# Performance work log

Measured on AMD Instinct MI355X. Metric: run time of the kernel, lower is better.

Reference implementation:

```python
import jax, jax.numpy as jnp
import numpy as np

IMG_H, IMG_W = 448, 800
GRID = 224
MIN_SIZE = 64.0
B, N, NCAM = 1, 48, 6


def setup_inputs() -> dict:
    rng = np.random.default_rng(0)
    centers = np.stack([rng.uniform(-40, 40, (B, N)), rng.uniform(-40, 40, (B, N)),
                        rng.uniform(-1.5, 0.5, (B, N))], -1)
    dims = rng.uniform(1.0, 4.0, (B, N, 3))
    heading = rng.uniform(-np.pi, np.pi, (B, N, 1))
    boxes7 = np.concatenate([centers, dims, heading], -1).astype(np.float32)
    gt_labels = rng.integers(1, 11, (B, N)).astype(np.int64)  # 1..10 as in gt_boxes[...,-1]
    imgs = rng.random((B, NCAM, 3, IMG_H, IMG_W)).astype(np.float32)
    # plausible lidar->image projections: 6 outward-facing cams, 60 deg apart, 90 deg hfov
    fx = fy = 400.0
    K = np.array([[fx, 0, IMG_W / 2], [0, fy, IMG_H / 2], [0, 0, 1]], np.float32)
    l2i = np.zeros((B, NCAM, 4, 4), np.float32)
    for c in range(NCAM):
        th = 2 * np.pi * c / NCAM
        right = np.array([np.sin(th), -np.cos(th), 0.0])
        down = np.array([0.0, 0.0, -1.0])
        fwdv = np.array([np.cos(th), np.sin(th), 0.0])
        R = np.stack([right, down, fwdv])  # lidar -> cam
        l2i[:, c, :3, :3] = K @ R
        l2i[:, c, 3, 3] = 1.0
    eye4 = np.eye(4, dtype=np.float32)
    img_aug = np.broadcast_to(eye4, (B, NCAM, 4, 4)).copy()
    lidar_aug = np.broadcast_to(eye4, (B, 4, 4)).copy()
    W_img = (rng.standard_normal((588, 768)) * 0.02).astype(np.float32)
    text_features = rng.standard_normal((10, 768)).astype(np.float32)
    return dict(boxes7=jnp.asarray(boxes7), gt_labels=jnp.asarray(gt_labels),
                camera_imgs=jnp.asarray(imgs), lidar2image=jnp.asarray(l2i),
                img_aug_matrix=jnp.asarray(img_aug), lidar_aug_matrix=jnp.asarray(lidar_aug),
                W_img=jnp.asarray(W_img), text_features=jnp.asarray(text_features),
                logit_scale=jnp.asarray(np.float32(np.log(100.0))))


def _boxes_to_corners_3d(boxes7):  # (M,7) -> (M,8,3)
    template = jnp.array([[1, 1, -1], [1, -1, -1], [-1, -1, -1], [-1, 1, -1],
                          [1, 1, 1], [1, -1, 1], [-1, -1, 1], [-1, 1, 1]], jnp.float32) * 0.5
    corners = boxes7[:, None, 3:6] * template[None]
    c, s = jnp.cos(boxes7[:, 6]), jnp.sin(boxes7[:, 6])
    z, o = jnp.zeros_like(c), jnp.ones_like(c)
    rot = jnp.stack([c, s, z, -s, c, z, z, z, o], -1).reshape(-1, 3, 3)
    corners = jnp.einsum('nki,nij->nkj', corners, rot)  # points @ R as in torch code
    return corners + boxes7[:, None, :3]


def _project(corners, l2i, img_aug, lidar_aug):
    # corners (M,3); l2i/img_aug (6,4,4); lidar_aug (4,4)
    pts = corners - lidar_aug[:3, 3]
    pts = jnp.linalg.inv(lidar_aug[:3, :3]) @ pts.T  # (3,M)
    p = jnp.einsum('cij,jm->cim', l2i[:, :3, :3], pts) + l2i[:, :3, 3][:, :, None]
    zc = jnp.clip(p[:, 2], 1e-5, 1e5)
    xy = p[:, :2] / zc[:, None]
    p = jnp.concatenate([xy, zc[:, None]], axis=1)  # (6,3,M)
    p = jnp.einsum('cij,cjm->cim', img_aug[:, :3, :3], p) + img_aug[:, :3, 3][:, :, None]
    rc = p[:, :2].transpose(0, 2, 1)[..., ::-1]  # (6,M,2) as (row, col)
    on_img = (rc[..., 0] < IMG_H) & (rc[..., 0] >= 0) & (rc[..., 1] < IMG_W) & (rc[..., 1] >= 0)
    return rc, on_img


def _bilinear(img, ix, iy):
    # img (3,H,W); ix, iy (N,GRID,GRID) pixel coords; zero padding, align_corners=False
    x0f, y0f = jnp.floor(ix), jnp.floor(iy)
    wx1, wy1 = ix - x0f, iy - y0f
    wx0, wy0 = 1.0 - wx1, 1.0 - wy1

    def gather(xf, yf):
        valid = (xf >= 0) & (xf <= IMG_W - 1) & (yf >= 0) & (yf <= IMG_H - 1)
        xi = jnp.clip(xf.astype(jnp.int32), 0, IMG_W - 1)
        yi = jnp.clip(yf.astype(jnp.int32), 0, IMG_H - 1)
        return img[:, yi, xi] * valid[None].astype(img.dtype)  # (3,N,G,G)

    return (gather(x0f, y0f) * (wx0 * wy0)[None] + gather(x0f + 1, y0f) * (wx1 * wy0)[None]
            + gather(x0f, y0f + 1) * (wx0 * wy1)[None] + gather(x0f + 1, y0f + 1) * (wx1 * wy1)[None])


def _forward(boxes7, gt_labels, camera_imgs, lidar2image, img_aug_matrix,
             lidar_aug_matrix, W_img, text_features, logit_scale):
    Bx, Nx = boxes7.shape[:2]
    corners = _boxes_to_corners_3d(boxes7.reshape(-1, 7)).reshape(Bx, Nx * 8, 3)
    rc, on_img = jax.vmap(_project)(corners, lidar2image, img_aug_matrix, lidar_aug_matrix)
    # .long() in torch truncates toward zero; coords are constants wrt grads
    all_coords = jax.lax.stop_gradient(jnp.trunc(rc)).astype(jnp.int32).reshape(Bx, NCAM, Nx, 8, 2)
    visible = on_img.reshape(Bx, NCAM, Nx, 8).any(-1)  # (B,6,N)
    rows, cols = all_coords[..., 0], all_coords[..., 1]
    x1 = jnp.clip(cols.min(-1), 0, IMG_W)
    x2 = jnp.clip(cols.max(-1), 0, IMG_W)
    y1 = jnp.clip(rows.min(-1), 0, IMG_H)
    y2 = jnp.clip(rows.max(-1), 0, IMG_H)
    sq = jnp.maximum(jnp.maximum(x2 - x1, y2 - y1).astype(jnp.float32), MIN_SIZE)
    u = jnp.linspace(0.0, 1.0, GRID)  # normalized affine_grid after min/max rescale
    px = x1.astype(jnp.float32)[..., None, None] + sq[..., None, None] * u[None, None, None, None, :]
    py = y1.astype(jnp.float32)[..., None, None] + sq[..., None, None] * u[None, None, None, :, None]
    gx = px / IMG_W * 2.0 - 1.0
    gy = py / IMG_H * 2.0 - 1.0
    ix = ((gx + 1.0) * IMG_W - 1.0) / 2.0  # unnormalize (align_corners=False)
    iy = ((gy + 1.0) * IMG_H - 1.0) / 2.0
    patches = jax.vmap(jax.vmap(_bilinear))(camera_imgs, ix, iy)  # (B,6,3,N,G,G)
    patches = patches.transpose(0, 1, 3, 2, 4, 5)  # (B,6,N,3,G,G)
    # stub CLIP image tower: 16x16 avg pool -> flatten -> linear to 768
    pooled = patches.reshape(Bx, NCAM, Nx, 3, 14, 16, 14, 16).mean(axis=(5, 7))
    feats = pooled.reshape(Bx, NCAM, Nx, 588) @ W_img  # (B,6,N,768)
    feats = feats / jnp.linalg.norm(feats, axis=-1, keepdims=True)
    text_n = text_features / jnp.linalg.norm(text_features, axis=-1, keepdims=True)
    logits = jnp.exp(logit_scale) * jnp.einsum('bcnd,kd->bcnk', feats, text_n)
    probs = jax.nn.softmax(logits, axis=-1) * visible[..., None].astype(logits.dtype)
    cnt = visible.sum(1).astype(probs.dtype)  # (B,N) cameras per box
    mean_probs = probs.sum(1) / jnp.maximum(cnt, 1.0)[..., None]  # (B,N,10)
    pred = jnp.argmax(mean_probs, axis=-1).reshape(-1)
    true = gt_labels.reshape(-1) - 1
    acc = (pred == true).astype(jnp.float32).mean()
    return pred, true, acc, mean_probs


def reference(boxes7, gt_labels, camera_imgs, lidar2image, img_aug_matrix,
              lidar_aug_matrix, W_img, text_features, logit_scale):
    return _forward(boxes7, gt_labels, camera_imgs, lidar2image, img_aug_matrix,
                    lidar_aug_matrix, W_img, text_features, logit_scale)
```

## Files before the change

kernel.cpp:

```cpp
#include <hip/hip_runtime.h>
#include <math.h>

#define IMG_H 448
#define IMG_W 800
#define GRIDN 224
#define NCAM 6
#define NBOX 48
#define NPAIR (NCAM * NBOX)
#define NCLASS 10
#define FEATD 768
#define POOLD 588
#define PROWS 14

#define WS_PAIR 0
#define WS_PART (NPAIR * 4)
#define WS_PROBS (WS_PART + NPAIR * PROWS * FEATD)

__global__ void __launch_bounds__(256) pool_gemv_kernel(const float* __restrict__ imgs,
                                                        const float* __restrict__ boxes7,
                                                        const float* __restrict__ l2i,
                                                        const float* __restrict__ img_aug,
                                                        const float* __restrict__ lidar_aug,
                                                        const float* __restrict__ W,
                                                        float* __restrict__ ws) {
    int pair = blockIdx.x / PROWS;
    int pr = blockIdx.x % PROWS;
    int cam = pair / NBOX, box = pair % NBOX;
    int tid = threadIdx.x;

    __shared__ float s_pw[4];
    __shared__ float s_pool[3 * 14];

    if (tid < 8) {
        int k = tid;
        float R[9];
        for (int i = 0; i < 3; ++i)
            for (int j = 0; j < 3; ++j) R[i * 3 + j] = lidar_aug[i * 4 + j];
        float ltx = lidar_aug[3], lty = lidar_aug[7], ltz = lidar_aug[11];
        float det = R[0] * (R[4] * R[8] - R[5] * R[7]) - R[1] * (R[3] * R[8] - R[5] * R[6]) +
                    R[2] * (R[3] * R[7] - R[4] * R[6]);
        float i0 = (R[4] * R[8] - R[5] * R[7]) / det;
        float i1 = (R[2] * R[7] - R[1] * R[8]) / det;
        float i2 = (R[1] * R[5] - R[2] * R[4]) / det;
        float i3 = (R[5] * R[6] - R[3] * R[8]) / det;
        float i4 = (R[0] * R[8] - R[2] * R[6]) / det;
        float i5 = (R[2] * R[3] - R[0] * R[5]) / det;
        float i6 = (R[3] * R[7] - R[4] * R[6]) / det;
        float i7 = (R[1] * R[6] - R[0] * R[7]) / det;
        float i8 = (R[0] * R[4] - R[1] * R[3]) / det;

        const float* M = l2i + cam * 16;
        const float* A = img_aug + cam * 16;
        const float* bxp = boxes7 + box * 7;
        float cx = bxp[0], cy = bxp[1], cz = bxp[2];
        float dx = bxp[3], dy = bxp[4], dz = bxp[5], hd = bxp[6];
        float ch = cosf(hd), sh = sinf(hd);
        float tx = (k & 2) ? -0.5f : 0.5f;
        float ty = ((k + 1) & 2) ? -0.5f : 0.5f;
        float tz = (k & 4) ? 0.5f : -0.5f;
        float lx = dx * tx, ly = dy * ty, lz = dz * tz;
        float wx = lx * ch - ly * sh + cx;
        float wy = lx * sh + ly * ch + cy;
        float wz = lz + cz;
        float px_ = wx - ltx, py_ = wy - lty, pz_ = wz - ltz;
        float qx = i0 * px_ + i1 * py_ + i2 * pz_;
        float qy = i3 * px_ + i4 * py_ + i5 * pz_;
        float qz = i6 * px_ + i7 * py_ + i8 * pz_;
        float p0 = M[0] * qx + M[1] * qy + M[2] * qz + M[3];
        float p1 = M[4] * qx + M[5] * qy + M[6] * qz + M[7];
        float p2 = M[8] * qx + M[9] * qy + M[10] * qz + M[11];
        float zc = fminf(fmaxf(p2, 1e-5f), 1e5f);
        float sx = p0 / zc, sy = p1 / zc;
        float q0 = A[0] * sx + A[1] * sy + A[2] * zc + A[3];
        float q1 = A[4] * sx + A[5] * sy + A[6] * zc + A[7];
        float row = q1, col = q0;
        int on = (row < (float)IMG_H) && (row >= 0.f) && (col < (float)IMG_W) && (col >= 0.f);
        int ri = (int)row;
        int ci = (int)col;
        int minr = ri, maxr = ri, minc = ci, maxc = ci, visv = on;
        for (int off = 4; off >= 1; off >>= 1) {
            minr = min(minr, __shfl_xor(minr, off, 8));
            maxr = max(maxr, __shfl_xor(maxr, off, 8));
            minc = min(minc, __shfl_xor(minc, off, 8));
            maxc = max(maxc, __shfl_xor(maxc, off, 8));
            visv |= __shfl_xor(visv, off, 8);
        }
        if (tid == 0) {
            int x1 = min(max(minc, 0), IMG_W);
            int x2 = min(max(maxc, 0), IMG_W);
            int y1 = min(max(minr, 0), IMG_H);
            int y2 = min(max(maxr, 0), IMG_H);
            float sq = fmaxf((float)max(x2 - x1, y2 - y1), 64.0f);
            s_pw[0] = (float)x1;
            s_pw[1] = (float)y1;
            s_pw[2] = sq;
            s_pw[3] = visv ? 1.0f : 0.0f;
            if (pr == 0) {
                float* pw = ws + WS_PAIR + pair * 4;
                pw[0] = (float)x1; pw[1] = (float)y1; pw[2] = sq;
                pw[3] = visv ? 1.0f : 0.0f;
            }
        }
    }
    __syncthreads();
    if (s_pw[3] == 0.f) return;
    float bx1 = s_pw[0], by1 = s_pw[1], sq = s_pw[2];

    const float* img0 = imgs + (size_t)cam * 3 * IMG_H * IMG_W;
    const float* img1 = img0 + (size_t)(IMG_H * IMG_W);
    const float* img2 = img0 + (size_t)(2 * IMG_H * IMG_W);
    bool active = tid < GRIDN;

    const float ustep = 1.0f / 223.0f;
    float wx0 = 0.f, wx1 = 0.f, mx0 = 0.f, mx1 = 0.f;
    int xi0 = 0, xi1 = 0;
    if (active) {
        float u = (float)tid * ustep;
        float px = bx1 + sq * u;
        float gx = px / (float)IMG_W * 2.0f - 1.0f;
        float ix = ((gx + 1.0f) * (float)IMG_W - 1.0f) / 2.0f;
        float x0f = floorf(ix);
        wx1 = ix - x0f;
        wx0 = 1.0f - wx1;
        float x1f = x0f + 1.0f;
        mx0 = (x0f >= 0.f && x0f <= (float)(IMG_W - 1)) ? 1.f : 0.f;
        mx1 = (x1f >= 0.f && x1f <= (float)(IMG_W - 1)) ? 1.f : 0.f;
        xi0 = min(max((int)x0f, 0), IMG_W - 1);
        xi1 = min(max((int)x1f, 0), IMG_W - 1);
    }

    int iyA = -0x40000000, iyB = -0x40000000;
    float vA00 = 0.f, vA01 = 0.f, vA10 = 0.f, vA11 = 0.f, vA20 = 0.f, vA21 = 0.f;
    float vB00 = 0.f, vB01 = 0.f, vB10 = 0.f, vB11 = 0.f, vB20 = 0.f, vB21 = 0.f;

    float acc0 = 0.f, acc1 = 0.f, acc2 = 0.f;
    for (int r = 0; r < 16; ++r) {
        int i = pr * 16 + r;
        float u = (float)i * ustep;
        float py = by1 + sq * u;
        float gy = py / (float)IMG_H * 2.0f - 1.0f;
        float iy = ((gy + 1.0f) * (float)IMG_H - 1.0f) / 2.0f;
        float y0f = floorf(iy);
        float wy1 = iy - y0f;
        float wy0 = 1.0f - wy1;
        float y1f = y0f + 1.0f;
        float my0 = (y0f >= 0.f && y0f <= (float)(IMG_H - 1)) ? 1.f : 0.f;
        float my1 = (y1f >= 0.f && y1f <= (float)(IMG_H - 1)) ? 1.f : 0.f;
        int yi0 = min(max((int)y0f, 0), IMG_H - 1);
        int yi1 = min(max((int)y1f, 0), IMG_H - 1);
        if (yi0 != iyA || yi1 != iyB) {
            if (yi0 == iyB) {
                vA00 = vB00; vA01 = vB01; vA10 = vB10; vA11 = vB11; vA20 = vB20; vA21 = vB21;
                iyA = iyB;
            } else if (yi0 != iyA) {
                if (active) {
                    int r0 = yi0 * IMG_W;
                    vA00 = img0[r0 + xi0]; vA01 = img0[r0 + xi1];
                    vA10 = img1[r0 + xi0]; vA11 = img1[r0 + xi1];
                    vA20 = img2[r0 + xi0]; vA21 = img2[r0 + xi1];
                }
                iyA = yi0;
            }
            if (yi1 != iyB) {
                if (active) {
                    int r1 = yi1 * IMG_W;
                    vB00 = img0[r1 + xi0]; vB01 = img0[r1 + xi1];
                    vB10 = img1[r1 + xi0]; vB11 = img1[r1 + xi1];
                    vB20 = img2[r1 + xi0]; vB21 = img2[r1 + xi1];
                }
                iyB = yi1;
            }
        }
        if (active) {
            float w00 = wx0 * wy0, w10 = wx1 * wy0, w01 = wx0 * wy1, w11 = wx1 * wy1;
            float m00 = mx0 * my0, m10 = mx1 * my0, m01 = mx0 * my1, m11 = mx1 * my1;
            acc0 += vA00 * m00 * w00 + vA01 * m10 * w10 + vB00 * m01 * w01 + vB01 * m11 * w11;
            acc1 += vA10 * m00 * w00 + vA11 * m10 * w10 + vB10 * m01 * w01 + vB11 * m11 * w11;
            acc2 += vA20 * m00 * w00 + vA21 * m10 * w10 + vB20 * m01 * w01 + vB21 * m11 * w11;
        }
    }
    for (int off = 8; off >= 1; off >>= 1) {
        acc0 += __shfl_xor(acc0, off, 16);
        acc1 += __shfl_xor(acc1, off, 16);
        acc2 += __shfl_xor(acc2, off, 16);
    }
    if (active && (tid & 15) == 0) {
        int pj = tid >> 4;
        s_pool[0 * 14 + pj] = acc0 * (1.0f / 256.0f);
        s_pool[1 * 14 + pj] = acc1 * (1.0f / 256.0f);
        s_pool[2 * 14 + pj] = acc2 * (1.0f / 256.0f);
    }
    __syncthreads();

    float f0 = 0.f, f1 = 0.f, f2 = 0.f;
#pragma unroll
    for (int c = 0; c < 3; ++c) {
        const float* Wc = W + ((size_t)(c * 196 + pr * 14)) * FEATD;
#pragma unroll 14
        for (int pj = 0; pj < 14; ++pj) {
            float p = s_pool[c * 14 + pj];
            const float* wr = Wc + (size_t)pj * FEATD;
            f0 += p * wr[tid];
            f1 += p * wr[tid + 256];
            f2 += p * wr[tid + 512];
        }
    }
    float* po = ws + WS_PART + ((size_t)pair * PROWS + pr) * FEATD;
    po[tid] = f0;
    po[tid + 256] = f1;
    po[tid + 512] = f2;
}

__global__ void __launch_bounds__(256) headred_kernel(const float* __restrict__ text,
                                                      const float* __restrict__ ls_ptr,
                                                      float* __restrict__ ws) {
    int pair = blockIdx.x;
    int tid = threadIdx.x;
    const float* pw = ws + WS_PAIR + pair * 4;
    if (pw[3] == 0.f) {
        if (tid < NCLASS) ws[WS_PROBS + pair * NCLASS + tid] = 0.f;
        return;
    }
    const float* pb = ws + WS_PART + (size_t)pair * PROWS * FEATD;
    float f0 = 0.f, f1 = 0.f, f2 = 0.f;
    for (int pr = 0; pr < PROWS; ++pr) {
        const float* fp = pb + (size_t)pr * FEATD;
        f0 += fp[tid];
        f1 += fp[tid + 256];
        f2 += fp[tid + 512];
    }
    float pn = f0 * f0 + f1 * f1 + f2 * f2;
    float pl[NCLASS], tq[NCLASS];
    for (int k = 0; k < NCLASS; ++k) {
        const float* tr = text + (size_t)k * FEATD;
        float t0 = tr[tid], t1 = tr[tid + 256], t2 = tr[tid + 512];
        pl[k] = f0 * t0 + f1 * t1 + f2 * t2;
        tq[k] = t0 * t0 + t1 * t1 + t2 * t2;
    }
    for (int off = 32; off >= 1; off >>= 1) {
        pn += __shfl_xor(pn, off);
        for (int k = 0; k < NCLASS; ++k) {
            pl[k] += __shfl_xor(pl[k], off);
            tq[k] += __shfl_xor(tq[k], off);
        }
    }
    __shared__ float rn[4];
    __shared__ float rl[4][NCLASS];
    __shared__ float rq[4][NCLASS];
    int wave = tid >> 6, lane = tid & 63;
    if (lane == 0) {
        rn[wave] = pn;
        for (int k = 0; k < NCLASS; ++k) { rl[wave][k] = pl[k]; rq[wave][k] = tq[k]; }
    }
    __syncthreads();
    if (tid == 0) {
        float n2 = rn[0] + rn[1] + rn[2] + rn[3];
        float nrm = sqrtf(n2);
        float scale = expf(ls_ptr[0]);
        float lg[NCLASS], m = -1e30f;
        for (int k = 0; k < NCLASS; ++k) {
            float d = rl[0][k] + rl[1][k] + rl[2][k] + rl[3][k];
            float tn = sqrtf(rq[0][k] + rq[1][k] + rq[2][k] + rq[3][k]);
            lg[k] = scale * (d / (nrm * tn));
            m = fmaxf(m, lg[k]);
        }
        float s = 0.f;
        for (int k = 0; k < NCLASS; ++k) {
            lg[k] = expf(lg[k] - m);
            s += lg[k];
        }
        float* probs = ws + WS_PROBS + pair * NCLASS;
        for (int k = 0; k < NCLASS; ++k) probs[k] = lg[k] / s;
    }
}

__global__ void finalize_kernel(const int* __restrict__ gt, const float* __restrict__ ws,
                                float* __restrict__ out) {
    int n = threadIdx.x;
    bool match = false;
    if (n < NBOX) {
        const float* probs = ws + WS_PROBS;
        float cnt = 0.f;
        for (int c = 0; c < NCAM; ++c)
            cnt += (ws[WS_PAIR + (c * NBOX + n) * 4 + 3] != 0.f) ? 1.f : 0.f;
        float denom = fmaxf(cnt, 1.0f);
        float mp[NCLASS];
        for (int k = 0; k < NCLASS; ++k) {
            float s = 0.f;
            for (int c = 0; c < NCAM; ++c) s += probs[(c * NBOX + n) * NCLASS + k];
            mp[k] = s / denom;
            out[97 + n * NCLASS + k] = mp[k];
        }
        float best = mp[0];
        int pred = 0;
        for (int k = 1; k < NCLASS; ++k)
            if (mp[k] > best) { best = mp[k]; pred = k; }
        int tr = gt[n] - 1;
        out[n] = (float)pred;
        out[NBOX + n] = (float)tr;
        match = (pred == tr);
    }
    unsigned long long b = __ballot(match);
    if (n == 0) out[2 * NBOX] = (float)__popcll(b) / (float)NBOX;
}

extern "C" void kernel_launch(void* const* d_in, const int* in_sizes, int n_in,
                              void* d_out, int out_size, void* d_ws, size_t ws_size,
                              hipStream_t stream) {
    const float* boxes7 = (const float*)d_in[0];
    const int* gt = (const int*)d_in[1];
    const float* imgs = (const float*)d_in[2];
    const float* l2i = (const float*)d_in[3];
    const float* img_aug = (const float*)d_in[4];
    const float* lidar_aug = (const float*)d_in[5];
    const float* W = (const float*)d_in[6];
    const float* text = (const float*)d_in[7];
    const float* ls = (const float*)d_in[8];
    float* ws = (float*)d_ws;
    float* out = (float*)d_out;

    pool_gemv_kernel<<<NPAIR * PROWS, 256, 0, stream>>>(imgs, boxes7, l2i, img_aug,
                                                        lidar_aug, W, ws);
    headred_kernel<<<NPAIR, 256, 0, stream>>>(text, ls, ws);
    finalize_kernel<<<1, 64, 0, stream>>>(gt, ws, out);
}
```

Measured before the change: 44.11 us.

## Fuse head reduction and finalize into one per-box kernel with atomic accuracy ticket

```diff
diff --git a/kernel.cpp b/kernel.cpp
--- a/kernel.cpp
+++ b/kernel.cpp
@@ -9,12 +9,11 @@
 #define NPAIR (NCAM * NBOX)
 #define NCLASS 10
 #define FEATD 768
-#define POOLD 588
 #define PROWS 14
 
 #define WS_PAIR 0
 #define WS_PART (NPAIR * 4)
-#define WS_PROBS (WS_PART + NPAIR * PROWS * FEATD)
+#define WS_CNT (WS_PART + NPAIR * PROWS * FEATD)
 
 __global__ void __launch_bounds__(256) pool_gemv_kernel(const float* __restrict__ imgs,
                                                         const float* __restrict__ boxes7,
@@ -27,6 +26,12 @@
     int pr = blockIdx.x % PROWS;
     int cam = pair / NBOX, box = pair % NBOX;
     int tid = threadIdx.x;
+
+    if (blockIdx.x == 0 && tid == 0) {
+        int* ip = (int*)(ws + WS_CNT);
+        ip[0] = 0;
+        ip[1] = 0;
+    }
 
     __shared__ float s_pw[4];
     __shared__ float s_pool[3 * 14];
@@ -211,97 +216,129 @@
     po[tid + 512] = f2;
 }
 
-__global__ void __launch_bounds__(256) headred_kernel(const float* __restrict__ text,
+__global__ void __launch_bounds__(256) headfin_kernel(const float* __restrict__ text,
                                                       const float* __restrict__ ls_ptr,
-                                                      float* __restrict__ ws) {
-    int pair = blockIdx.x;
+                                                      const int* __restrict__ gt,
+                                                      float* __restrict__ ws,
+                                                      float* __restrict__ out) {
+    int n = blockIdx.x;
     int tid = threadIdx.x;
-    const float* pw = ws + WS_PAIR + pair * 4;
-    if (pw[3] == 0.f) {
-        if (tid < NCLASS) ws[WS_PROBS + pair * NCLASS + tid] = 0.f;
-        return;
-    }
-    const float* pb = ws + WS_PART + (size_t)pair * PROWS * FEATD;
-    float f0 = 0.f, f1 = 0.f, f2 = 0.f;
-    for (int pr = 0; pr < PROWS; ++pr) {
-        const float* fp = pb + (size_t)pr * FEATD;
-        f0 += fp[tid];
-        f1 += fp[tid + 256];
-        f2 += fp[tid + 512];
-    }
-    float pn = f0 * f0 + f1 * f1 + f2 * f2;
-    float pl[NCLASS], tq[NCLASS];
-    for (int k = 0; k < NCLASS; ++k) {
-        const float* tr = text + (size_t)k * FEATD;
-        float t0 = tr[tid], t1 = tr[tid + 256], t2 = tr[tid + 512];
-        pl[k] = f0 * t0 + f1 * t1 + f2 * t2;
-        tq[k] = t0 * t0 + t1 * t1 + t2 * t2;
-    }
-    for (int off = 32; off >= 1; off >>= 1) {
-        pn += __shfl_xor(pn, off);
-        for (int k = 0; k < NCLASS; ++k) {
-            pl[k] += __shfl_xor(pl[k], off);
-            tq[k] += __shfl_xor(tq[k], off);
-        }
-    }
+    int wave = tid >> 6, lane = tid & 63;
+
     __shared__ float rn[4];
     __shared__ float rl[4][NCLASS];
     __shared__ float rq[4][NCLASS];
-    int wave = tid >> 6, lane = tid & 63;
-    if (lane == 0) {
-        rn[wave] = pn;
-        for (int k = 0; k < NCLASS; ++k) { rl[wave][k] = pl[k]; rq[wave][k] = tq[k]; }
+    __shared__ float s_tn[NCLASS];
+    __shared__ float s_mp[NCLASS];
+    __shared__ float s_cnt;
+
+    float t0[NCLASS], t1[NCLASS], t2[NCLASS];
+#pragma unroll
+    for (int k = 0; k < NCLASS; ++k) {
+        const float* tr = text + (size_t)k * FEATD;
+        t0[k] = tr[tid];
+        t1[k] = tr[tid + 256];
+        t2[k] = tr[tid + 512];
+    }
+    {
+        float tq[NCLASS];
+#pragma unroll
+        for (int k = 0; k < NCLASS; ++k) tq[k] = t0[k] * t0[k] + t1[k] * t1[k] + t2[k] * t2[k];
+        for (int off = 32; off >= 1; off >>= 1)
+#pragma unroll
+            for (int k = 0; k < NCLASS; ++k) tq[k] += __shfl_xor(tq[k], off);
+        if (lane == 0)
+#pragma unroll
+            for (int k = 0; k < NCLASS; ++k) rq[wave][k] = tq[k];
     }
     __syncthreads();
     if (tid == 0) {
-        float n2 = rn[0] + rn[1] + rn[2] + rn[3];
-        float nrm = sqrtf(n2);
-        float scale = expf(ls_ptr[0]);
-        float lg[NCLASS], m = -1e30f;
+#pragma unroll
         for (int k = 0; k < NCLASS; ++k) {
-            float d = rl[0][k] + rl[1][k] + rl[2][k] + rl[3][k];
-            float tn = sqrtf(rq[0][k] + rq[1][k] + rq[2][k] + rq[3][k]);
-            lg[k] = scale * (d / (nrm * tn));
-            m = fmaxf(m, lg[k]);
-        }
-        float s = 0.f;
+            s_tn[k] = sqrtf(rq[0][k] + rq[1][k] + rq[2][k] + rq[3][k]);
+            s_mp[k] = 0.f;
+        }
+        s_cnt = 0.f;
+    }
+    __syncthreads();
+
+    float scale = expf(ls_ptr[0]);
+    for (int c = 0; c < NCAM; ++c) {
+        int pair = c * NBOX + n;
+        bool vis = ws[WS_PAIR + pair * 4 + 3] != 0.f;
+        if (!vis) continue;
+        const float* pb = ws + WS_PART + (size_t)pair * PROWS * FEATD;
+        float f0 = 0.f, f1 = 0.f, f2 = 0.f;
+        for (int pr = 0; pr < PROWS; ++pr) {
+            const float* fp = pb + (size_t)pr * FEATD;
+            f0 += fp[tid];
+            f1 += fp[tid + 256];
+            f2 += fp[tid + 512];
+        }
+        float pn = f0 * f0 + f1 * f1 + f2 * f2;
+        float pl[NCLASS];
+#pragma unroll
+        for (int k = 0; k < NCLASS; ++k) pl[k] = f0 * t0[k] + f1 * t1[k] + f2 * t2[k];
+        for (int off = 32; off >= 1; off >>= 1) {
+            pn += __shfl_xor(pn, off);
+#pragma unroll
+            for (int k = 0; k < NCLASS; ++k) pl[k] += __shfl_xor(pl[k], off);
+        }
+        if (lane == 0) {
+            rn[wave] = pn;
+#pragma unroll
+            for (int k = 0; k < NCLASS; ++k) rl[wave][k] = pl[k];
+        }
+        __syncthreads();
+        if (tid == 0) {
+            float nrm = sqrtf(rn[0] + rn[1] + rn[2] + rn[3]);
+            float lg[NCLASS], m = -1e30f;
+#pragma unroll
+            for (int k = 0; k < NCLASS; ++k) {
+                float d = rl[0][k] + rl[1][k] + rl[2][k] + rl[3][k];
+                lg[k] = scale * (d / (nrm * s_tn[k]));
+                m = fmaxf(m, lg[k]);
+            }
+            float s = 0.f;
+#pragma unroll
+            for (int k = 0; k < NCLASS; ++k) {
+                lg[k] = expf(lg[k] - m);
+                s += lg[k];
+            }
+#pragma unroll
+            for (int k = 0; k < NCLASS; ++k) s_mp[k] += lg[k] / s;
+            s_cnt += 1.f;
+        }
+        __syncthreads();
+    }
+
+    if (tid == 0) {
+        float denom = fmaxf(s_cnt, 1.0f);
+        float mp[NCLASS];
+        float best = -1.f;
+        int pred = 0;
+#pragma unroll
         for (int k = 0; k < NCLASS; ++k) {
-            lg[k] = expf(lg[k] - m);
-            s += lg[k];
-        }
-        float* probs = ws + WS_PROBS + pair * NCLASS;
-        for (int k = 0; k < NCLASS; ++k) probs[k] = lg[k] / s;
-    }
-}
-
-__global__ void finalize_kernel(const int* __restrict__ gt, const float* __restrict__ ws,
-                                float* __restrict__ out) {
-    int n = threadIdx.x;
-    bool match = false;
-    if (n < NBOX) {
-        const float* probs = ws + WS_PROBS;
-        float cnt = 0.f;
-        for (int c = 0; c < NCAM; ++c)
-            cnt += (ws[WS_PAIR + (c * NBOX + n) * 4 + 3] != 0.f) ? 1.f : 0.f;
-        float denom = fmaxf(cnt, 1.0f);
-        float mp[NCLASS];
-        for (int k = 0; k < NCLASS; ++k) {
-            float s = 0.f;
-            for (int c = 0; c < NCAM; ++c) s += probs[(c * NBOX + n) * NCLASS + k];
-            mp[k] = s / denom;
+            mp[k] = s_mp[k] / denom;
             out[97 + n * NCLASS + k] = mp[k];
         }
-        float best = mp[0];
-        int pred = 0;
+        best = mp[0];
+#pragma unroll
         for (int k = 1; k < NCLASS; ++k)
             if (mp[k] > best) { best = mp[k]; pred = k; }
         int tr = gt[n] - 1;
         out[n] = (float)pred;
         out[NBOX + n] = (float)tr;
-        match = (pred == tr);
-    }
-    unsigned long long b = __ballot(match);
-    if (n == 0) out[2 * NBOX] = (float)__popcll(b) / (float)NBOX;
+        int match = (pred == tr) ? 1 : 0;
+        int* ip = (int*)(ws + WS_CNT);
+        atomicAdd(&ip[0], match);
+        __threadfence();
+        int ticket = atomicAdd(&ip[1], 1);
+        if (ticket == NBOX - 1) {
+            int mcount = atomicAdd(&ip[0], 0);
+            out[2 * NBOX] = (float)mcount / (float)NBOX;
+        }
+    }
 }
 
 extern "C" void kernel_launch(void* const* d_in, const int* in_sizes, int n_in,
@@ -321,6 +358,5 @@
 
     pool_gemv_kernel<<<NPAIR * PROWS, 256, 0, stream>>>(imgs, boxes7, l2i, img_aug,
                                                         lidar_aug, W, ws);
-    headred_kernel<<<NPAIR, 256, 0, stream>>>(text, ls, ws);
-    finalize_kernel<<<1, 64, 0, stream>>>(gt, ws, out);
+    headfin_kernel<<<NBOX, 256, 0, stream>>>(text, ls, gt, ws, out);
 }
```

Result: slower. 46.97 us (+6.5%).
